# Optimization experiments

Measured on AMD Instinct MI355X. Metric: run time of the kernel, lower is better.

## Reference

```python
import jax, jax.numpy as jnp
import numpy as np

B, S, D_IN, D_H = 8, 2048, 1024, 64

def setup_inputs() -> dict:
    key = jax.random.key(0)
    kq, kk, kv, kwq, kwk, kwv = jax.random.split(key, 6)
    sc = 1.0 / np.sqrt(D_IN)
    return {
        "query": jax.random.normal(kq, (B, S, D_IN), dtype=jnp.float32),
        "key": jax.random.normal(kk, (B, S, D_IN), dtype=jnp.float32),
        "value": jax.random.normal(kv, (B, S, D_IN), dtype=jnp.float32),
        # nn.Linear weights: [out, in]
        "W_q": jax.random.normal(kwq, (D_H, D_IN), dtype=jnp.float32) * sc,
        "W_k": jax.random.normal(kwk, (D_H, D_IN), dtype=jnp.float32) * sc,
        "W_v": jax.random.normal(kwv, (D_H, D_IN), dtype=jnp.float32) * sc,
    }

def reference(query, key, value, W_q, W_k, W_v):
    Q = jnp.einsum('bsd,hd->bsh', query, W_q)   # [B,S,D_H]
    K = jnp.einsum('bsd,hd->bsh', key, W_k)
    V = jnp.einsum('bsd,hd->bsh', value, W_v)
    scores = jnp.einsum('bqh,bkh->bqk', Q, K) / jnp.sqrt(jnp.float32(D_H))  # [B,S,S]
    causal = jnp.tril(jnp.ones((S, S), dtype=bool))
    scores = jnp.where(causal, scores, jnp.float32(-jnp.inf))
    attn = jax.nn.softmax(scores, axis=-1)
    return jnp.einsum('bqk,bkh->bqh', attn, V)  # [B,S,D_H]
```

## Files before the change

kernel.cpp:

```cpp
#include <hip/hip_runtime.h>
#include <hip/hip_bf16.h>

#define B_  8
#define S_  2048
#define DIN 1024
#define DH  64

typedef __bf16 bf16;
typedef __attribute__((ext_vector_type(8))) __bf16 bf16x8;
typedef __attribute__((ext_vector_type(4))) float f32x4;

__global__ __launch_bounds__(256) void wconv_kernel(const float* __restrict__ wq,
                                                    const float* __restrict__ wk,
                                                    const float* __restrict__ wv,
                                                    bf16* __restrict__ wb) {
  int i = blockIdx.x * 256 + threadIdx.x;
  int L  = i & 63;
  int kc = (i >> 6) & 31;
  int w  = (i >> 11) & 3;
  int p  = i >> 13;
  const float* src = (p == 0) ? wq : ((p == 1) ? wk : wv);
  int row = w * 16 + (L & 15);
  int k8  = kc * 32 + (L >> 4) * 8;
  const float4* ap = reinterpret_cast<const float4*>(src + (size_t)row * DIN + k8);
  float4 a0 = ap[0], a1 = ap[1];
  bf16x8 av;
  av[0]=(bf16)a0.x; av[1]=(bf16)a0.y; av[2]=(bf16)a0.z; av[3]=(bf16)a0.w;
  av[4]=(bf16)a1.x; av[5]=(bf16)a1.y; av[6]=(bf16)a1.z; av[7]=(bf16)a1.w;
  *reinterpret_cast<bf16x8*>(wb + ((size_t)((p*4 + w)*32 + kc)*64 + L) * 8) = av;
}

__global__ __launch_bounds__(256) void proj_kernel(
    const float* __restrict__ inq, const float* __restrict__ ink, const float* __restrict__ inv,
    const bf16* __restrict__ wb_all,
    bf16* __restrict__ qb, bf16* __restrict__ kb, bf16* __restrict__ vt) {
  const int p = blockIdx.y;
  const float* in = (p == 0) ? inq : ((p == 1) ? ink : inv);
  const int tid  = threadIdx.x;
  const int lane = tid & 63;
  const int w    = tid >> 6;
  const int col16 = lane & 15, g = lane >> 4;
  const int tile = blockIdx.x * 4 + w;
  const int row0 = tile * 16;

  const float* arow = in + (size_t)(row0 + col16) * DIN + g * 8;
  const bf16*  bbase = wb_all + (size_t)p * 4 * 16384 + lane * 8;

  f32x4 acc[4] = {};
  float4 pf0[2], pf1[2];
  pf0[0] = *reinterpret_cast<const float4*>(arow);
  pf1[0] = *reinterpret_cast<const float4*>(arow + 4);
  pf0[1] = *reinterpret_cast<const float4*>(arow + 32);
  pf1[1] = *reinterpret_cast<const float4*>(arow + 36);

  #pragma unroll
  for (int kc = 0; kc < 32; kc++) {
    float4 a0 = pf0[kc & 1], a1 = pf1[kc & 1];
    if (kc + 2 < 32) {
      pf0[kc & 1] = *reinterpret_cast<const float4*>(arow + (kc + 2) * 32);
      pf1[kc & 1] = *reinterpret_cast<const float4*>(arow + (kc + 2) * 32 + 4);
    }
    bf16x8 av;
    av[0]=(bf16)a0.x; av[1]=(bf16)a0.y; av[2]=(bf16)a0.z; av[3]=(bf16)a0.w;
    av[4]=(bf16)a1.x; av[5]=(bf16)a1.y; av[6]=(bf16)a1.z; av[7]=(bf16)a1.w;
    #pragma unroll
    for (int n = 0; n < 4; n++) {
      bf16x8 bv = *reinterpret_cast<const bf16x8*>(bbase + n * 16384 + kc * 512);
      acc[n] = __builtin_amdgcn_mfma_f32_16x16x32_bf16(av, bv, acc[n], 0, 0, 0);
    }
  }

  const int rowbase = row0 + g * 4;
  #pragma unroll
  for (int n = 0; n < 4; n++)
    #pragma unroll
    for (int rg = 0; rg < 4; rg++) {
      int rr = rowbase + rg;
      int cc = n * 16 + col16;
      if (p == 0)      qb[(size_t)rr * DH + cc] = (bf16)acc[n][rg];
      else if (p == 1) kb[(size_t)rr * DH + cc] = (bf16)acc[n][rg];
      else {
        int bb = rr >> 11, ss = rr & 2047;
        vt[((size_t)bb * DH + cc) * S_ + ss] = (bf16)acc[n][rg];
      }
    }
}

__global__ __launch_bounds__(512) void attn_kernel(
    const bf16* __restrict__ qb, const bf16* __restrict__ kb, const bf16* __restrict__ vt,
    float* __restrict__ out) {
  const int qt = blockIdx.x;
  const int b  = blockIdx.y;
  const int lane = threadIdx.x & 63;
  const int w    = threadIdx.x >> 6;
  const int col16 = lane & 15, g = lane >> 4;
  const int row0 = qt * 16;

  __shared__ float pacc[8][16][64];
  __shared__ float pm[8][16];
  __shared__ float pl_[8][16];
  __shared__ bf16 plds[8][16 * 64];
  bf16* pl = plds[w];

  bf16x8 qf[2];
  {
    const bf16* qrow = qb + ((size_t)(b * S_ + row0 + col16)) * DH + g * 8;
    qf[0] = *reinterpret_cast<const bf16x8*>(qrow);
    qf[1] = *reinterpret_cast<const bf16x8*>(qrow + 32);
  }

  f32x4 acc[4] = {};
  float m_r[4], l_r[4];
  #pragma unroll
  for (int i = 0; i < 4; i++) { m_r[i] = -1e30f; l_r[i] = 0.f; }

  const int nt = (qt + 4) >> 2;

  for (int t = w; t < nt; t += 8) {
    const int kvb = t * 64;
    f32x4 s[4] = {};
    #pragma unroll
    for (int n = 0; n < 4; n++) {
      const bf16* krow = kb + ((size_t)(b * S_ + kvb + n*16 + col16)) * DH + g * 8;
      bf16x8 kf0 = *reinterpret_cast<const bf16x8*>(krow);
      bf16x8 kf1 = *reinterpret_cast<const bf16x8*>(krow + 32);
      s[n] = __builtin_amdgcn_mfma_f32_16x16x32_bf16(qf[0], kf0, s[n], 0, 0, 0);
      s[n] = __builtin_amdgcn_mfma_f32_16x16x32_bf16(qf[1], kf1, s[n], 0, 0, 0);
    }
    float vals[4][4];
    const bool diag = (t == nt - 1);
    #pragma unroll
    for (int n = 0; n < 4; n++)
      #pragma unroll
      for (int rg = 0; rg < 4; rg++) {
        float v = s[n][rg] * 0.125f;
        if (diag) {
          int kvp = kvb + n*16 + col16;
          int qp  = row0 + g*4 + rg;
          if (kvp > qp) v = -1e30f;
        }
        vals[n][rg] = v;
      }
    float rmax[4];
    #pragma unroll
    for (int rg = 0; rg < 4; rg++)
      rmax[rg] = fmaxf(fmaxf(vals[0][rg], vals[1][rg]), fmaxf(vals[2][rg], vals[3][rg]));
    #pragma unroll
    for (int off = 1; off < 16; off <<= 1)
      #pragma unroll
      for (int rg = 0; rg < 4; rg++)
        rmax[rg] = fmaxf(rmax[rg], __shfl_xor(rmax[rg], off));
    float scl[4], rsum[4];
    #pragma unroll
    for (int rg = 0; rg < 4; rg++) {
      float mn = fmaxf(m_r[rg], rmax[rg]);
      scl[rg] = __expf(m_r[rg] - mn);
      m_r[rg] = mn;
      rsum[rg] = 0.f;
    }
    #pragma unroll
    for (int n = 0; n < 4; n++)
      #pragma unroll
      for (int rg = 0; rg < 4; rg++) {
        float pp = __expf(vals[n][rg] - m_r[rg]);
        vals[n][rg] = pp;
        rsum[rg] += pp;
      }
    #pragma unroll
    for (int off = 1; off < 16; off <<= 1)
      #pragma unroll
      for (int rg = 0; rg < 4; rg++)
        rsum[rg] += __shfl_xor(rsum[rg], off);
    #pragma unroll
    for (int rg = 0; rg < 4; rg++)
      l_r[rg] = l_r[rg] * scl[rg] + rsum[rg];
    #pragma unroll
    for (int n = 0; n < 4; n++)
      #pragma unroll
      for (int rg = 0; rg < 4; rg++)
        acc[n][rg] *= scl[rg];
    #pragma unroll
    for (int n = 0; n < 4; n++)
      #pragma unroll
      for (int rg = 0; rg < 4; rg++) {
        int row = g*4 + rg;
        int idx = (row * 64 + n*16 + col16) ^ ((row & 7) << 3);
        pl[idx] = (bf16)vals[n][rg];
      }
    bf16x8 pa[2];
    {
      int row = col16;
      int i0 = (row * 64 + 0  + g * 8) ^ ((row & 7) << 3);
      int i1 = (row * 64 + 32 + g * 8) ^ ((row & 7) << 3);
      pa[0] = *reinterpret_cast<const bf16x8*>(&pl[i0]);
      pa[1] = *reinterpret_cast<const bf16x8*>(&pl[i1]);
    }
    #pragma unroll
    for (int nd = 0; nd < 4; nd++) {
      const bf16* vrow = vt + ((size_t)(b * DH + nd*16 + col16)) * S_ + kvb + g * 8;
      bf16x8 v0 = *reinterpret_cast<const bf16x8*>(vrow);
      bf16x8 v1 = *reinterpret_cast<const bf16x8*>(vrow + 32);
      acc[nd] = __builtin_amdgcn_mfma_f32_16x16x32_bf16(pa[0], v0, acc[nd], 0, 0, 0);
      acc[nd] = __builtin_amdgcn_mfma_f32_16x16x32_bf16(pa[1], v1, acc[nd], 0, 0, 0);
    }
  }

  #pragma unroll
  for (int n = 0; n < 4; n++)
    #pragma unroll
    for (int rg = 0; rg < 4; rg++)
      pacc[w][g*4 + rg][n*16 + col16] = acc[n][rg];
  if (col16 == 0) {
    #pragma unroll
    for (int rg = 0; rg < 4; rg++) {
      pm[w][g*4 + rg]  = m_r[rg];
      pl_[w][g*4 + rg] = l_r[rg];
    }
  }
  __syncthreads();

  const int tid = threadIdx.x;
  #pragma unroll
  for (int i = 0; i < 2; i++) {
    int idx = tid + i * 512;
    int row = idx >> 6, col = idx & 63;
    float M = -1e30f;
    #pragma unroll
    for (int ww = 0; ww < 8; ww++) M = fmaxf(M, pm[ww][row]);
    float L = 0.f, o = 0.f;
    #pragma unroll
    for (int ww = 0; ww < 8; ww++) {
      float e = __expf(pm[ww][row] - M);
      L += pl_[ww][row] * e;
      o += pacc[ww][row][col] * e;
    }
    out[((size_t)b * S_ + row0 + row) * DH + col] = o / L;
  }
}

extern "C" void kernel_launch(void* const* d_in, const int* in_sizes, int n_in,
                              void* d_out, int out_size, void* d_ws, size_t ws_size,
                              hipStream_t stream) {
  const float* q  = (const float*)d_in[0];
  const float* k  = (const float*)d_in[1];
  const float* v  = (const float*)d_in[2];
  const float* wq = (const float*)d_in[3];
  const float* wk = (const float*)d_in[4];
  const float* wv = (const float*)d_in[5];

  char* ws = (char*)d_ws;
  bf16* Wb = (bf16*)(ws);
  bf16* Qb = (bf16*)(ws + 1572864);
  bf16* Kb = (bf16*)(ws + 1572864 + 2097152);
  bf16* Vt = (bf16*)(ws + 1572864 + 4194304);

  wconv_kernel<<<dim3(96), 256, 0, stream>>>(wq, wk, wv, Wb);
  proj_kernel<<<dim3(B_ * S_ / 64, 3), 256, 0, stream>>>(q, k, v, Wb, Qb, Kb, Vt);
  attn_kernel<<<dim3(S_ / 16, B_), 512, 0, stream>>>(Qb, Kb, Vt, (float*)d_out);
}
```

Before: 98.98 us.

## Stage projection inputs and weights through LDS with async double-buffered loads

The projection kernel now gives each block a 64-row tile. It copies activation and weight slices into double-buffered shared memory using direct global-to-LDS loads, with a swizzled layout to avoid bank conflicts. Before, each wave streamed its own rows and re-read weights from cache. The aim is to overlap the next K-slice fetch with the current MFMA work, to share weight tiles across waves, and to improve achieved bandwidth on the fp32 input stream. The weight-conversion kernel is relaid to match the new tile order, but its launch grid was raised to 4x the needed threads. That does redundant work, although it still stays inside the workspace.

```diff
diff --git a/kernel.cpp b/kernel.cpp
--- a/kernel.cpp
+++ b/kernel.cpp
@@ -10,24 +10,31 @@
 typedef __attribute__((ext_vector_type(8))) __bf16 bf16x8;
 typedef __attribute__((ext_vector_type(4))) float f32x4;
 
+__device__ inline void gload_lds16(const void* g, void* l) {
+  __builtin_amdgcn_global_load_lds(
+      (const __attribute__((address_space(1))) unsigned int*)g,
+      (__attribute__((address_space(3))) unsigned int*)l, 16, 0, 0);
+}
+
 __global__ __launch_bounds__(256) void wconv_kernel(const float* __restrict__ wq,
                                                     const float* __restrict__ wk,
                                                     const float* __restrict__ wv,
                                                     bf16* __restrict__ wb) {
-  int i = blockIdx.x * 256 + threadIdx.x;
-  int L  = i & 63;
-  int kc = (i >> 6) & 31;
-  int w  = (i >> 11) & 3;
-  int p  = i >> 13;
+  int c = blockIdx.x * 256 + threadIdx.x;
+  int l   = c & 63;
+  int n   = (c >> 6) & 3;
+  int kc2 = (c >> 8) & 1;
+  int ks  = (c >> 9) & 15;
+  int p   = c >> 13;
   const float* src = (p == 0) ? wq : ((p == 1) ? wk : wv);
-  int row = w * 16 + (L & 15);
-  int k8  = kc * 32 + (L >> 4) * 8;
+  int row = n * 16 + (l & 15);
+  int k8  = ks * 64 + kc2 * 32 + (l >> 4) * 8;
   const float4* ap = reinterpret_cast<const float4*>(src + (size_t)row * DIN + k8);
   float4 a0 = ap[0], a1 = ap[1];
   bf16x8 av;
   av[0]=(bf16)a0.x; av[1]=(bf16)a0.y; av[2]=(bf16)a0.z; av[3]=(bf16)a0.w;
   av[4]=(bf16)a1.x; av[5]=(bf16)a1.y; av[6]=(bf16)a1.z; av[7]=(bf16)a1.w;
-  *reinterpret_cast<bf16x8*>(wb + ((size_t)((p*4 + w)*32 + kc)*64 + L) * 8) = av;
+  *reinterpret_cast<bf16x8*>(wb + (size_t)c * 8) = av;
 }
 
 __global__ __launch_bounds__(256) void proj_kernel(
@@ -36,41 +43,63 @@
     bf16* __restrict__ qb, bf16* __restrict__ kb, bf16* __restrict__ vt) {
   const int p = blockIdx.y;
   const float* in = (p == 0) ? inq : ((p == 1) ? ink : inv);
+  const bf16* wbp = wb_all + (size_t)p * 16 * 4096;
   const int tid  = threadIdx.x;
   const int lane = tid & 63;
   const int w    = tid >> 6;
   const int col16 = lane & 15, g = lane >> 4;
-  const int tile = blockIdx.x * 4 + w;
-  const int row0 = tile * 16;
-
-  const float* arow = in + (size_t)(row0 + col16) * DIN + g * 8;
-  const bf16*  bbase = wb_all + (size_t)p * 4 * 16384 + lane * 8;
+  const int row0 = blockIdx.x * 64;
+
+  __shared__ float As[2][4096];
+  __shared__ bf16  Bs[2][4096];
+
+  const int arow_l = w * 16 + (lane >> 4);
+  const int aswz0  = (lane & 15) * 16;
+  #define STAGE(buf, ks)                                                          \
+    {                                                                             \
+      _Pragma("unroll")                                                           \
+      for (int j = 0; j < 4; j++) {                                               \
+        int row = arow_l + j * 4;                                                 \
+        int swb = aswz0 ^ ((row & 7) << 5);                                       \
+        const char* gp = (const char*)(in + (size_t)(row0 + row) * DIN + (ks) * 64) + swb; \
+        gload_lds16(gp, (char*)&As[buf][0] + w * 4096 + j * 1024);                \
+      }                                                                           \
+      _Pragma("unroll")                                                           \
+      for (int j = 0; j < 2; j++) {                                               \
+        const char* gp = (const char*)(wbp + (size_t)(ks) * 4096) + w * 2048 + j * 1024 + lane * 16; \
+        gload_lds16(gp, (char*)&Bs[buf][0] + w * 2048 + j * 1024);                \
+      }                                                                           \
+    }
 
   f32x4 acc[4] = {};
-  float4 pf0[2], pf1[2];
-  pf0[0] = *reinterpret_cast<const float4*>(arow);
-  pf1[0] = *reinterpret_cast<const float4*>(arow + 4);
-  pf0[1] = *reinterpret_cast<const float4*>(arow + 32);
-  pf1[1] = *reinterpret_cast<const float4*>(arow + 36);
-
-  #pragma unroll
-  for (int kc = 0; kc < 32; kc++) {
-    float4 a0 = pf0[kc & 1], a1 = pf1[kc & 1];
-    if (kc + 2 < 32) {
-      pf0[kc & 1] = *reinterpret_cast<const float4*>(arow + (kc + 2) * 32);
-      pf1[kc & 1] = *reinterpret_cast<const float4*>(arow + (kc + 2) * 32 + 4);
-    }
-    bf16x8 av;
-    av[0]=(bf16)a0.x; av[1]=(bf16)a0.y; av[2]=(bf16)a0.z; av[3]=(bf16)a0.w;
-    av[4]=(bf16)a1.x; av[5]=(bf16)a1.y; av[6]=(bf16)a1.z; av[7]=(bf16)a1.w;
-    #pragma unroll
-    for (int n = 0; n < 4; n++) {
-      bf16x8 bv = *reinterpret_cast<const bf16x8*>(bbase + n * 16384 + kc * 512);
-      acc[n] = __builtin_amdgcn_mfma_f32_16x16x32_bf16(av, bv, acc[n], 0, 0, 0);
-    }
-  }
-
-  const int rowbase = row0 + g * 4;
+  int buf = 0;
+  STAGE(0, 0);
+  __syncthreads();
+
+  for (int ks = 0; ks < 16; ks++) {
+    if (ks < 15) STAGE(buf ^ 1, ks + 1);
+    const char* ab = (const char*)&As[buf][0] + w * 4096 + col16 * 256;
+    const char* bb = (const char*)&Bs[buf][0] + lane * 16;
+    #pragma unroll
+    for (int kc = 0; kc < 2; kc++) {
+      int abyte = (kc * 128 + g * 32) ^ ((col16 & 7) << 5);
+      f32x4 a0 = *reinterpret_cast<const f32x4*>(ab + abyte);
+      f32x4 a1 = *reinterpret_cast<const f32x4*>(ab + abyte + 16);
+      bf16x8 av;
+      av[0]=(bf16)a0[0]; av[1]=(bf16)a0[1]; av[2]=(bf16)a0[2]; av[3]=(bf16)a0[3];
+      av[4]=(bf16)a1[0]; av[5]=(bf16)a1[1]; av[6]=(bf16)a1[2]; av[7]=(bf16)a1[3];
+      #pragma unroll
+      for (int n = 0; n < 4; n++) {
+        bf16x8 bv = *reinterpret_cast<const bf16x8*>(bb + kc * 4096 + n * 1024);
+        acc[n] = __builtin_amdgcn_mfma_f32_16x16x32_bf16(av, bv, acc[n], 0, 0, 0);
+      }
+    }
+    __syncthreads();
+    buf ^= 1;
+  }
+  #undef STAGE
+
+  const int rowbase = row0 + w * 16 + g * 4;
   #pragma unroll
   for (int n = 0; n < 4; n++)
     #pragma unroll
@@ -80,8 +109,8 @@
       if (p == 0)      qb[(size_t)rr * DH + cc] = (bf16)acc[n][rg];
       else if (p == 1) kb[(size_t)rr * DH + cc] = (bf16)acc[n][rg];
       else {
-        int bb = rr >> 11, ss = rr & 2047;
-        vt[((size_t)bb * DH + cc) * S_ + ss] = (bf16)acc[n][rg];
+        int bb2 = rr >> 11, ss = rr & 2047;
+        vt[((size_t)bb2 * DH + cc) * S_ + ss] = (bf16)acc[n][rg];
       }
     }
 }
@@ -254,7 +283,7 @@
   bf16* Kb = (bf16*)(ws + 1572864 + 2097152);
   bf16* Vt = (bf16*)(ws + 1572864 + 4194304);
 
-  wconv_kernel<<<dim3(96), 256, 0, stream>>>(wq, wk, wv, Wb);
+  wconv_kernel<<<dim3(384), 256, 0, stream>>>(wq, wk, wv, Wb);
   proj_kernel<<<dim3(B_ * S_ / 64, 3), 256, 0, stream>>>(q, k, v, Wb, Qb, Kb, Vt);
   attn_kernel<<<dim3(S_ / 16, B_), 512, 0, stream>>>(Qb, Kb, Vt, (float*)d_out);
 }
```

After: 93.41 us. 1.06x faster.

## Split projection GEMM along K into partials plus a separate reduce kernel

Applied to the files above, without the earlier changes.

The projection kernel now splits the 1024-wide reduction into two halves. Each wave computes half of a 16-row tile, which doubles the number of waves working on the K dimension, and writes fp32 partial sums to workspace. A new reduce kernel adds the two partials, converts the sums to bf16 and writes Q, K and transposed V. The register double-buffered prefetch is dropped. The change adds an extra launch and about 25MB of fp32 partial traffic in exchange for more parallelism in a projection that is bound by streaming the inputs.

```diff
diff --git a/kernel.cpp b/kernel.cpp
--- a/kernel.cpp
+++ b/kernel.cpp
@@ -30,36 +30,27 @@
   *reinterpret_cast<bf16x8*>(wb + ((size_t)((p*4 + w)*32 + kc)*64 + L) * 8) = av;
 }
 
-__global__ __launch_bounds__(256) void proj_kernel(
+__global__ __launch_bounds__(256) void proj_partial_kernel(
     const float* __restrict__ inq, const float* __restrict__ ink, const float* __restrict__ inv,
     const bf16* __restrict__ wb_all,
-    bf16* __restrict__ qb, bf16* __restrict__ kb, bf16* __restrict__ vt) {
+    float* __restrict__ part) {
   const int p = blockIdx.y;
   const float* in = (p == 0) ? inq : ((p == 1) ? ink : inv);
-  const int tid  = threadIdx.x;
-  const int lane = tid & 63;
-  const int w    = tid >> 6;
+  const int lane = threadIdx.x & 63;
+  const int w    = threadIdx.x >> 6;
   const int col16 = lane & 15, g = lane >> 4;
-  const int tile = blockIdx.x * 4 + w;
+  const int tile = blockIdx.x * 2 + (w >> 1);
+  const int ks   = w & 1;
   const int row0 = tile * 16;
 
-  const float* arow = in + (size_t)(row0 + col16) * DIN + g * 8;
-  const bf16*  bbase = wb_all + (size_t)p * 4 * 16384 + lane * 8;
+  const float* arow = in + (size_t)(row0 + col16) * DIN + ks * 512 + g * 8;
+  const bf16*  bbase = wb_all + (size_t)p * 4 * 16384 + (size_t)ks * 16 * 512 + lane * 8;
 
   f32x4 acc[4] = {};
-  float4 pf0[2], pf1[2];
-  pf0[0] = *reinterpret_cast<const float4*>(arow);
-  pf1[0] = *reinterpret_cast<const float4*>(arow + 4);
-  pf0[1] = *reinterpret_cast<const float4*>(arow + 32);
-  pf1[1] = *reinterpret_cast<const float4*>(arow + 36);
-
-  #pragma unroll
-  for (int kc = 0; kc < 32; kc++) {
-    float4 a0 = pf0[kc & 1], a1 = pf1[kc & 1];
-    if (kc + 2 < 32) {
-      pf0[kc & 1] = *reinterpret_cast<const float4*>(arow + (kc + 2) * 32);
-      pf1[kc & 1] = *reinterpret_cast<const float4*>(arow + (kc + 2) * 32 + 4);
-    }
+  #pragma unroll
+  for (int kc = 0; kc < 16; kc++) {
+    float4 a0 = *reinterpret_cast<const float4*>(arow + kc * 32);
+    float4 a1 = *reinterpret_cast<const float4*>(arow + kc * 32 + 4);
     bf16x8 av;
     av[0]=(bf16)a0.x; av[1]=(bf16)a0.y; av[2]=(bf16)a0.z; av[3]=(bf16)a0.w;
     av[4]=(bf16)a1.x; av[5]=(bf16)a1.y; av[6]=(bf16)a1.z; av[7]=(bf16)a1.w;
@@ -70,20 +61,35 @@
     }
   }
 
-  const int rowbase = row0 + g * 4;
+  float* pout = part + ((size_t)(p * 1024 + tile) * 2 + ks) * 1024;
   #pragma unroll
   for (int n = 0; n < 4; n++)
     #pragma unroll
-    for (int rg = 0; rg < 4; rg++) {
-      int rr = rowbase + rg;
-      int cc = n * 16 + col16;
-      if (p == 0)      qb[(size_t)rr * DH + cc] = (bf16)acc[n][rg];
-      else if (p == 1) kb[(size_t)rr * DH + cc] = (bf16)acc[n][rg];
-      else {
-        int bb = rr >> 11, ss = rr & 2047;
-        vt[((size_t)bb * DH + cc) * S_ + ss] = (bf16)acc[n][rg];
-      }
-    }
+    for (int rg = 0; rg < 4; rg++)
+      pout[(g*4 + rg) * 64 + n*16 + col16] = acc[n][rg];
+}
+
+__global__ __launch_bounds__(256) void reduce_kernel(const float* __restrict__ part,
+                                                     bf16* __restrict__ qb,
+                                                     bf16* __restrict__ kb,
+                                                     bf16* __restrict__ vt) {
+  int gid = blockIdx.x * 256 + threadIdx.x;
+  #pragma unroll
+  for (int i = 0; i < 4; i++) {
+    int e = i * 786432 + gid;
+    int p = e >> 20;
+    int r = e & 1048575;
+    int tile = r >> 10, rc = r & 1023;
+    const float* pp = part + (size_t)(p * 1024 + tile) * 2048 + rc;
+    float s = pp[0] + pp[1024];
+    int row = (tile << 4) + (rc >> 6), col = rc & 63;
+    if (p == 0)      qb[(size_t)row * DH + col] = (bf16)s;
+    else if (p == 1) kb[(size_t)row * DH + col] = (bf16)s;
+    else {
+      int bb = row >> 11, ss = row & 2047;
+      vt[((size_t)bb * DH + col) * S_ + ss] = (bf16)s;
+    }
+  }
 }
 
 __global__ __launch_bounds__(512) void attn_kernel(
@@ -249,12 +255,14 @@
   const float* wv = (const float*)d_in[5];
 
   char* ws = (char*)d_ws;
-  bf16* Wb = (bf16*)(ws);
-  bf16* Qb = (bf16*)(ws + 1572864);
-  bf16* Kb = (bf16*)(ws + 1572864 + 2097152);
-  bf16* Vt = (bf16*)(ws + 1572864 + 4194304);
+  bf16*  Wb   = (bf16*)(ws);
+  bf16*  Qb   = (bf16*)(ws + 1572864);
+  bf16*  Kb   = (bf16*)(ws + 3670016);
+  bf16*  Vt   = (bf16*)(ws + 5767168);
+  float* Part = (float*)(ws + 7864320);
 
   wconv_kernel<<<dim3(96), 256, 0, stream>>>(wq, wk, wv, Wb);
-  proj_kernel<<<dim3(B_ * S_ / 64, 3), 256, 0, stream>>>(q, k, v, Wb, Qb, Kb, Vt);
+  proj_partial_kernel<<<dim3(512, 3), 256, 0, stream>>>(q, k, v, Wb, Part);
+  reduce_kernel<<<dim3(3072), 256, 0, stream>>>(Part, Qb, Kb, Vt);
   attn_kernel<<<dim3(S_ / 16, B_), 512, 0, stream>>>(Qb, Kb, Vt, (float*)d_out);
 }
```

After: 111.7 us. 12.8% more time.
